# Kernel optimization log

Hardware: AMD Instinct MI355X
Metric: run time of the kernel (lower is better)

## Reference

```python
import jax, jax.numpy as jnp
from jax import lax
import numpy as np

N_HOS, N_TYPES, N_STRUCTS = 4, 16, 512
N_COMBOS = N_HOS * N_TYPES  # 64
HID = 1024
N_ITERS = 60  # fixed PDHG iterations (differentiable unrolled solver)


def setup_inputs() -> dict:
    key = jax.random.key(0)
    ks = jax.random.split(key, 8)
    X = jax.random.uniform(ks[0], (2048, N_HOS, N_TYPES), dtype=jnp.float32)
    # sparse 0/1 structure matrix; guarantee each structure touches >=1 combo
    S = (jax.random.uniform(ks[1], (N_COMBOS, N_STRUCTS)) < 0.08).astype(jnp.float32)
    cols = jnp.arange(N_STRUCTS)
    S = S.at[cols % N_COMBOS, cols].set(1.0)
    # MLP params (He-ish init)
    W1 = jax.random.normal(ks[2], (N_COMBOS, HID), dtype=jnp.float32) * (2.0 / N_COMBOS) ** 0.5
    b1 = jnp.zeros((HID,), jnp.float32)
    W2 = jax.random.normal(ks[3], (HID, HID), dtype=jnp.float32) * (2.0 / HID) ** 0.5
    b2 = jnp.zeros((HID,), jnp.float32)
    W3 = jax.random.normal(ks[4], (HID, N_STRUCTS), dtype=jnp.float32) * (2.0 / HID) ** 0.5
    b3 = jnp.zeros((N_STRUCTS,), jnp.float32)
    return {"X": X, "W1": W1, "b1": b1, "W2": W2, "b2": b2,
            "W3": W3, "b3": b3, "S": S, "batch_size": 2048}


def nn_forward(X, W1, b1, W2, b2, W3, b3):
    # torch loop applies act_fun after EVERY layer, including the last
    Z = X.reshape(X.shape[0], -1)                 # [B, n_hos*n_types]
    Z = jax.nn.relu(Z @ W1 + b1)
    Z = jax.nn.relu(Z @ W2 + b2)
    Z = jax.nn.relu(Z @ W3 + b3)                  # [B, n_structures]
    return Z


def solve_lp(S, W, B, Z, n_iters=N_ITERS):
    """Batched solve of: max_x W.x - ||x - Z||_2  s.t. x >= 0, S x <= B.
    PDHG (Chambolle-Pock) on  min_x f(x) + i{Kx <= c},
    f(x) = -W.x + ||x - Z||_2,  K = [S; -I],  c = [B; 0].
    Same optimization problem as the CvxpyLayer, solved by a fixed-iteration
    batched primal-dual method (differentiable via unrolling)."""
    batch, n = Z.shape
    m = S.shape[0]

    # ||K||_2 via power iteration on K^T K = S^T S + I (constant wrt params)
    def pow_step(v, _):
        v2 = S.T @ (S @ v) + v
        return v2 / jnp.linalg.norm(v2), None
    v0 = jnp.full((n,), 1.0 / np.sqrt(n), Z.dtype)
    v, _ = lax.scan(pow_step, v0, None, length=30)
    L = jnp.sqrt(jnp.vdot(v, S.T @ (S @ v) + v))
    L = lax.stop_gradient(L)
    tau = 0.9 / L
    sigma = 0.9 / L

    c = jnp.concatenate([B, jnp.zeros_like(Z)], axis=-1)  # [B, m+n]

    def Kx(x):
        return jnp.concatenate([x @ S.T, -x], axis=-1)    # [B, m+n]

    def KTy(y):
        return y[:, :m] @ S - y[:, m:]                    # [B, n]

    def prox_f(v):
        # argmin_x 1/(2 tau) ||x - v||^2 - W.x + ||x - Z||_2
        u = v + tau * W
        d = u - Z
        nrm = jnp.linalg.norm(d, axis=-1, keepdims=True)
        scale = jnp.maximum(1.0 - tau / jnp.maximum(nrm, 1e-12), 0.0)
        return Z + scale * d

    def step(carry, _):
        x, xbar, y = carry
        y = jnp.maximum(y + sigma * (Kx(xbar) - c), 0.0)
        x_new = prox_f(x - tau * KTy(y))
        xbar = 2.0 * x_new - x
        return (x_new, xbar, y), None

    x0 = jnp.zeros_like(Z)
    y0 = jnp.zeros((batch, m + n), Z.dtype)
    (x, _, _), _ = lax.scan(step, (x0, x0, y0), None, length=n_iters)
    return x


def reference(X, W1, b1, W2, b2, W3, b3, S, batch_size):
    Z = nn_forward(X, W1, b1, W2, b2, W3, b3)     # [B, n_structures]
    W = jnp.ones_like(Z)                          # weights w = 1 (as in torch)
    B = X.reshape(batch_size, -1)                 # capacities b
    return solve_lp(S, W, B, Z)
```

## Files before the change

### kernel.cpp

```cpp
#include <hip/hip_runtime.h>


typedef _Float16 half8 __attribute__((ext_vector_type(8)));
typedef __fp16 fp16x2 __attribute__((ext_vector_type(2)));
typedef __fp16 fp16x4 __attribute__((ext_vector_type(4)));
typedef float floatx4 __attribute__((ext_vector_type(4)));
typedef float floatx2 __attribute__((ext_vector_type(2)));

#define BATCH 2048
#define NITERS 60
#define XBS 520
#define YLS 72

typedef const __attribute__((address_space(1))) unsigned int* gptr_as1;
typedef __attribute__((address_space(3))) unsigned int* lptr_as3;
__device__ __forceinline__ void gl_lds16(const _Float16* g, _Float16* s) {
    __builtin_amdgcn_global_load_lds((gptr_as1)g, (lptr_as3)s, 16, 0, 0);
}
__device__ __forceinline__ floatx2 pmax0(floatx2 a) {
    return __builtin_elementwise_max(a, floatx2{0.f, 0.f});
}

template <int CTRL>
__device__ __forceinline__ float dpp_addf(float x) {
    int y = __builtin_amdgcn_update_dpp(0, __builtin_bit_cast(int, x), CTRL, 0xf, 0xf, true);
    return x + __builtin_bit_cast(float, y);
}
__device__ __forceinline__ float sum16(float x) {
    x = dpp_addf<0xB1>(x);
    x = dpp_addf<0x4E>(x);
    x = dpp_addf<0x124>(x);
    x = dpp_addf<0x128>(x);
    return x;
}
__device__ __forceinline__ float sum64(float x) {
    x = sum16(x);
    x += __builtin_bit_cast(float, __builtin_amdgcn_ds_swizzle(__builtin_bit_cast(int, x), 0x401F));
    x += __shfl_xor(x, 32, 64);
    return x;
}

__device__ void power_64(const float* __restrict__ S, float* __restrict__ tau_g) {
    __shared__ unsigned long long rowm[64][8];
    __shared__ float G[64][65];
    __shared__ float wl[64], pg[4][64];
    int t = threadIdx.x, wv = t >> 6, ln = t & 63;
    for (int rr = 0; rr < 16; rr++) {
        int r = wv * 16 + rr;
        float v[8];
#pragma unroll
        for (int e = 0; e < 8; e++) v[e] = S[r * 512 + e * 64 + ln];
#pragma unroll
        for (int e = 0; e < 8; e++) {
            unsigned long long m = __ballot(v[e] != 0.f);
            if (ln == 0) rowm[r][e] = m;
        }
    }
    __syncthreads();
    for (int k = 0; k < 16; k++) {
        int idx = t * 16 + k;
        int i = idx >> 6, j = idx & 63;
        int cnt = 0;
#pragma unroll
        for (int e = 0; e < 8; e++) cnt += __popcll(rowm[i][e] & rowm[j][e]);
        G[i][j] = (float)cnt;
    }
    if (wv == 0) {
        int cnt = 0;
#pragma unroll
        for (int e = 0; e < 8; e++) cnt += __popcll(rowm[ln][e]);
        wl[ln] = (float)cnt * 0.044194173824159216f;
    }
    __syncthreads();
    for (int s = 0; s < 30; s++) {
        float a = 0.f;
#pragma unroll
        for (int jj = 0; jj < 16; jj++) {
            int j = wv * 16 + jj;
            a += G[ln][j] * wl[j];
        }
        pg[wv][ln] = a;
        __syncthreads();
        if (wv == 0) {
            float g = (pg[0][ln] + pg[1][ln]) + (pg[2][ln] + pg[3][ln]);
            float wi = wl[ln];
            float s1 = sum64(wi * g);
            float s2 = sum64(wi * wi);
            float n = sqrtf(s1 + 2.f * s2 + 1.f);
            wl[ln] = (g + wi) / n;
        }
        __syncthreads();
    }
    if (wv == 0) {
        float wi = wl[ln];
        float s2 = sum64(wi * wi);
        if (ln == 0) tau_g[0] = 0.9f / sqrtf(s2 + 1.f);
    }
}

__global__ __launch_bounds__(256) void prep(
    const float* __restrict__ X, _Float16* __restrict__ Xh,
    const float* __restrict__ W1, _Float16* __restrict__ W1t,
    const float* __restrict__ W2, _Float16* __restrict__ W2t,
    const float* __restrict__ W3, _Float16* __restrict__ W3t,
    const float* __restrict__ S, _Float16* __restrict__ s1f,
    _Float16* __restrict__ s2f) {
    __shared__ float tile[32][33];
    int tid = threadIdx.x;
    int bid = blockIdx.x;
    if (bid < 512) {
        int i = bid * 256 + tid;
        Xh[i] = (_Float16)X[i];
        return;
    }
    bid -= 512;
    if (bid < 1600) {
        const float* W; _Float16* Wt; int K, N, b;
        if (bid < 64)        { W = W1; Wt = W1t; K = 64;   N = 1024; b = bid; }
        else if (bid < 1088) { W = W2; Wt = W2t; K = 1024; N = 1024; b = bid - 64; }
        else                 { W = W3; Wt = W3t; K = 1024; N = 512;  b = bid - 1088; }
        int nbx = N / 32;
        int n0 = (b % nbx) * 32, k0 = (b / nbx) * 32;
        int tx = tid & 31, ty = tid >> 5;
#pragma unroll
        for (int i = 0; i < 4; i++)
            tile[ty + i * 8][tx] = W[(size_t)(k0 + ty + i * 8) * N + n0 + tx];
        __syncthreads();
#pragma unroll
        for (int i = 0; i < 4; i++)
            Wt[(size_t)(n0 + ty + i * 8) * K + k0 + tx] = (_Float16)tile[tx][ty + i * 8];
        return;
    }
    bid -= 1600;
    int i = bid * 256 + tid;
    if (i < 4 * 16 * 64 * 8) {
        int j = i & 7, lane = (i >> 3) & 63, kk = (i >> 9) & 15, wc = i >> 13;
        int p = kk * 32 + (lane >> 4) * 8 + j;
        int lmc = (p & 127) >> 3, tc = p & 7;
        int c = (p >> 7) * 128 + tc * 16 + lmc;
        int m = wc * 16 + (lane & 15);
        s1f[i] = (_Float16)S[m * 512 + c];
    } else {
        int i2 = i - 4 * 16 * 64 * 8;
        int j = i2 & 7, lane = (i2 >> 3) & 63, c = (i2 >> 9) & 1,
            tt = (i2 >> 10) & 7, wc = i2 >> 13;
        int kc = c * 32 + (lane >> 4) * 8 + j;
        int n = wc * 128 + tt * 16 + (lane & 15);
        s2f[i2] = (_Float16)S[kc * 512 + n];
    }
}

__global__ __launch_bounds__(256) void gemm_relu(
    const _Float16* __restrict__ A, const _Float16* __restrict__ Wt,
    const float* __restrict__ bias, _Float16* __restrict__ outh,
    float* __restrict__ outf, int N, int K,
    const float* __restrict__ Sp, float* __restrict__ tau_g) {
    __shared__ __align__(16) _Float16 As[128 * 32];
    __shared__ __align__(16) _Float16 Bs[64 * 32];
    int tid = threadIdx.x;
    int bm = blockIdx.y * 128;
    int bn = blockIdx.x * 64;
    if (bn >= N) {
        if (blockIdx.y == 0 && Sp) power_64(Sp, tau_g);
        return;
    }
    int w = tid >> 6, l = tid & 63;
    int wr = w >> 1, wc = w & 1;
    int lm = l & 15, q = l >> 4;
    floatx4 acc[4][2] = {};

    int sr = l >> 2;
    int sc = (l & 3) * 8;
    const _Float16* ag0 = A + (size_t)(bm + w * 32 + sr) * K + sc;
    const _Float16* ag1 = A + (size_t)(bm + w * 32 + 16 + sr) * K + sc;
    _Float16* as0 = &As[(w * 32) * 32];
    _Float16* as1 = &As[(w * 32 + 16) * 32];
    const _Float16* bg = Wt + (size_t)(bn + w * 16 + sr) * K + sc;
    _Float16* bs = &Bs[(w * 16) * 32];

    for (int k0 = 0; k0 < K; k0 += 32) {
        gl_lds16(ag0 + k0, as0);
        gl_lds16(ag1 + k0, as1);
        gl_lds16(bg + k0, bs);
        __syncthreads();
        half8 af[4], bf[2];
#pragma unroll
        for (int mt = 0; mt < 4; mt++)
            af[mt] = *(const half8*)&As[(wr * 64 + mt * 16 + lm) * 32 + q * 8];
#pragma unroll
        for (int nt = 0; nt < 2; nt++)
            bf[nt] = *(const half8*)&Bs[(wc * 32 + nt * 16 + lm) * 32 + q * 8];
#pragma unroll
        for (int mt = 0; mt < 4; mt++)
#pragma unroll
            for (int nt = 0; nt < 2; nt++)
                acc[mt][nt] = __builtin_amdgcn_mfma_f32_16x16x32_f16(
                    af[mt], bf[nt], acc[mt][nt], 0, 0, 0);
        __syncthreads();
    }
#pragma unroll
    for (int nt = 0; nt < 2; nt++) {
        int col = bn + wc * 32 + nt * 16 + lm;
        float bv = bias[col];
#pragma unroll
        for (int mt = 0; mt < 4; mt++) {
#pragma unroll
            for (int v = 0; v < 4; v++) {
                int row = bm + wr * 64 + mt * 16 + q * 4 + v;
                float val = fmaxf(acc[mt][nt][v] + bv, 0.f);
                if (outh) outh[(size_t)row * N + col] = (_Float16)val;
                else      outf[(size_t)row * N + col] = val;
            }
        }
    }
}

__global__ __launch_bounds__(512, 2) void pdhg_mfma(
    const float* __restrict__ Zb, const float* __restrict__ Xf,
    const _Float16* __restrict__ s1f, const _Float16* __restrict__ s2f,
    const float* __restrict__ tau_p, float* __restrict__ out) {
    __shared__ __align__(16) _Float16 xb_d[16 * XBS];
    __shared__ __align__(16) _Float16 yl_d[16 * YLS];
    __shared__ __align__(16) float red[16][8];
    int tid = threadIdx.x;
    int wave = tid >> 6, p = wave >> 1, s = wave & 1;
    int l = tid & 63, lm = l & 15, q = l >> 4;
    int b0 = blockIdx.x * 8;
    bool act = (q < 2);

    half8 s1[16], s2[4][2];
#pragma unroll
    for (int k = 0; k < 16; k++)
        s1[k] = *(const half8*)&s1f[((p * 16 + k) * 64 + l) * 8];
#pragma unroll
    for (int tt = 0; tt < 4; tt++)
#pragma unroll
        for (int c = 0; c < 2; c++)
            s2[tt][c] = *(const half8*)&s2f[(((p * 8 + s * 4 + tt) * 2 + c) * 64 + l) * 8];

    floatx2 z2[2][4], x2[2][4], xb2[2][4], yh2[2][4], d2[2][4];
    floatx2 ylo2[2], Bc2[2];
    floatx4 a1p[4] = {};
    floatx4 acc2[4] = {};
    float tau = tau_p[0];
    float sig = tau;
#pragma unroll
    for (int vp = 0; vp < 2; vp++) {
        int r0 = b0 + ((q * 4 + 2 * vp) & 7);
        int r1 = b0 + ((q * 4 + 2 * vp + 1) & 7);
        Bc2[vp] = floatx2{Xf[r0 * 64 + p * 16 + lm], Xf[r1 * 64 + p * 16 + lm]};
        ylo2[vp] = floatx2{0.f, 0.f};
#pragma unroll
        for (int tt = 0; tt < 4; tt++) {
            int cc = p * 128 + (s * 4 + tt) * 16 + lm;
            z2[vp][tt] = floatx2{Zb[(size_t)r0 * 512 + cc], Zb[(size_t)r1 * 512 + cc]};
            x2[vp][tt] = floatx2{0.f, 0.f};
            xb2[vp][tt] = floatx2{0.f, 0.f};
            yh2[vp][tt] = floatx2{0.f, 0.f};
        }
    }
    {
        half8 hz = {0, 0, 0, 0, 0, 0, 0, 0};
        for (int i = tid; i < (16 * XBS) / 8; i += 512)
            *(half8*)&xb_d[i * 8] = hz;
        for (int i = tid; i < 16 * YLS; i += 512)
            yl_d[i] = (_Float16)0.f;
    }
    __syncthreads();

#pragma unroll 1
    for (int it = 0; it < NITERS; ++it) {
#pragma unroll
        for (int k = 0; k < 16; k++) {
            half8 ad = *(const half8*)&xb_d[lm * XBS + k * 32 + q * 8];
            a1p[k & 3] = __builtin_amdgcn_mfma_f32_16x16x32_f16(ad, s1[k], a1p[k & 3], 0, 0, 0);
        }
        floatx4 a1 = (a1p[0] + a1p[1]) + (a1p[2] + a1p[3]);
#pragma unroll
        for (int vp = 0; vp < 2; vp++) {
            floatx2 av = (vp == 0) ? floatx2{a1.x, a1.y} : floatx2{a1.z, a1.w};
            floatx2 yv = pmax0(ylo2[vp] + sig * (av - Bc2[vp]));
            floatx2 dy = yv - ylo2[vp];
            ylo2[vp] = yv;
            if (act && vp == s) {
                fp16x2 pk = __builtin_amdgcn_cvt_pkrtz(dy.x, dy.y);
                int a0 = (q * 4 + 2 * vp) * YLS + p * 16 + lm;
                yl_d[a0] = (_Float16)pk[0];
                yl_d[a0 + YLS] = (_Float16)pk[1];
            }
        }
        __syncthreads();
        half8 a2d[2];
#pragma unroll
        for (int c = 0; c < 2; c++)
            a2d[c] = *(const half8*)&yl_d[lm * YLS + c * 32 + q * 8];
#pragma unroll
        for (int tt = 0; tt < 4; tt++)
#pragma unroll
            for (int c = 0; c < 2; c++)
                acc2[tt] = __builtin_amdgcn_mfma_f32_16x16x32_f16(a2d[c], s2[tt][c], acc2[tt], 0, 0, 0);
        floatx2 pn2[2] = {floatx2{0.f, 0.f}, floatx2{0.f, 0.f}};
#pragma unroll
        for (int vp = 0; vp < 2; vp++)
#pragma unroll
            for (int tt = 0; tt < 4; tt++) {
                floatx2 accp = (vp == 0) ? floatx2{acc2[tt].x, acc2[tt].y}
                                         : floatx2{acc2[tt].z, acc2[tt].w};
                yh2[vp][tt] = pmax0(yh2[vp][tt] - sig * xb2[vp][tt]);
                floatx2 kty = accp - yh2[vp][tt];
                floatx2 dd = (x2[vp][tt] - tau * kty) + (tau - z2[vp][tt]);
                d2[vp][tt] = dd;
                pn2[vp] += dd * dd;
            }
        float pn[4] = {pn2[0].x, pn2[0].y, pn2[1].x, pn2[1].y};
#pragma unroll
        for (int v = 0; v < 4; v++) pn[v] = sum16(pn[v]);
        if (lm == 0)
#pragma unroll
            for (int v = 0; v < 4; v++) red[q * 4 + v][wave] = pn[v];
        __syncthreads();
        floatx2 sc2[2];
#pragma unroll
        for (int vp = 0; vp < 2; vp++)
#pragma unroll
            for (int c = 0; c < 2; c++) {
                int v = 2 * vp + c;
                floatx4 r0 = *(const floatx4*)&red[q * 4 + v][0];
                floatx4 r1 = *(const floatx4*)&red[q * 4 + v][4];
                floatx4 rr = r0 + r1;
                float n2 = (rr.x + rr.y) + (rr.z + rr.w);
                float sv = fmaxf(1.f - tau * rsqrtf(fmaxf(n2, 1e-24f)), 0.f);
                if (c == 0) sc2[vp].x = sv; else sc2[vp].y = sv;
            }
#pragma unroll
        for (int vp = 0; vp < 2; vp++) {
#pragma unroll
            for (int tt = 0; tt < 4; tt++) {
                floatx2 xn = z2[vp][tt] + sc2[vp] * d2[vp][tt];
                floatx2 xbn = 2.f * xn - x2[vp][tt];
                d2[vp][tt] = xbn - xb2[vp][tt];
                x2[vp][tt] = xn;
                xb2[vp][tt] = xbn;
            }
            if (act) {
#pragma unroll
                for (int c = 0; c < 2; c++) {
                    fp16x2 p0 = __builtin_amdgcn_cvt_pkrtz(
                        (c == 0) ? d2[vp][0].x : d2[vp][0].y,
                        (c == 0) ? d2[vp][1].x : d2[vp][1].y);
                    fp16x2 p1 = __builtin_amdgcn_cvt_pkrtz(
                        (c == 0) ? d2[vp][2].x : d2[vp][2].y,
                        (c == 0) ? d2[vp][3].x : d2[vp][3].y);
                    fp16x4 hd = __builtin_shufflevector(p0, p1, 0, 1, 2, 3);
                    int v = 2 * vp + c;
                    *(fp16x4*)&xb_d[(q * 4 + v) * XBS + p * 128 + lm * 8 + s * 4] = hd;
                }
            }
        }
        __syncthreads();
    }
    if (act)
#pragma unroll
        for (int vp = 0; vp < 2; vp++)
#pragma unroll
            for (int tt = 0; tt < 4; tt++) {
                int cc = p * 128 + (s * 4 + tt) * 16 + lm;
                out[(size_t)(b0 + q * 4 + 2 * vp) * 512 + cc] = x2[vp][tt].x;
                out[(size_t)(b0 + q * 4 + 2 * vp + 1) * 512 + cc] = x2[vp][tt].y;
            }
}

extern "C" void kernel_launch(void* const* d_in, const int* in_sizes, int n_in,
                              void* d_out, int out_size, void* d_ws, size_t ws_size,
                              hipStream_t stream) {
    const float* X  = (const float*)d_in[0];
    const float* W1 = (const float*)d_in[1];
    const float* b1 = (const float*)d_in[2];
    const float* W2 = (const float*)d_in[3];
    const float* b2 = (const float*)d_in[4];
    const float* W3 = (const float*)d_in[5];
    const float* b3 = (const float*)d_in[6];
    const float* S  = (const float*)d_in[7];
    float* out = (float*)d_out;

    char* ws = (char*)d_ws;
    size_t off = 0;
    auto alloc = [&](size_t bytes) {
        void* p = ws + off;
        off += (bytes + 255) & ~(size_t)255;
        return p;
    };
    _Float16* Xh  = (_Float16*)alloc((size_t)BATCH * 64 * 2);
    _Float16* W1t = (_Float16*)alloc((size_t)64 * 1024 * 2);
    _Float16* W2t = (_Float16*)alloc((size_t)1024 * 1024 * 2);
    _Float16* W3t = (_Float16*)alloc((size_t)1024 * 512 * 2);
    _Float16* H1  = (_Float16*)alloc((size_t)BATCH * 1024 * 2);
    _Float16* H2  = (_Float16*)alloc((size_t)BATCH * 1024 * 2);
    float*    Zb  = (float*)alloc((size_t)BATCH * 512 * 4);
    _Float16* s1f = (_Float16*)alloc((size_t)4 * 16 * 64 * 8 * 2);
    _Float16* s2f = (_Float16*)alloc((size_t)4 * 8 * 2 * 64 * 8 * 2);
    float*    tau = (float*)alloc(256);

    hipLaunchKernelGGL(prep, dim3(2368), dim3(256), 0, stream,
                       X, Xh, W1, W1t, W2, W2t, W3, W3t, S, s1f, s2f);
    hipLaunchKernelGGL(gemm_relu, dim3(16, 16), dim3(256), 0, stream,
                       Xh, W1t, b1, H1, (float*)nullptr, 1024, 64,
                       (const float*)nullptr, (float*)nullptr);
    hipLaunchKernelGGL(gemm_relu, dim3(17, 16), dim3(256), 0, stream,
                       H1, W2t, b2, H2, (float*)nullptr, 1024, 1024, S, tau);
    hipLaunchKernelGGL(gemm_relu, dim3(8, 16), dim3(256), 0, stream,
                       H2, W3t, b3, (_Float16*)nullptr, Zb, 512, 1024,
                       (const float*)nullptr, (float*)nullptr);
    hipLaunchKernelGGL(pdhg_mfma, dim3(BATCH / 8), dim3(512), 0, stream,
                       Zb, X, s1f, s2f, tau, out);
}
```

Measured before the change: 231.2 us.

## Restructure PDHG kernel to four waves per block with full MFMA row use

The PDHG solver block shrinks from 8 waves to 4 waves (256 threads). Each wave now owns a full 128-column slice and computes all 8 second-stage MFMA tiles. Previously half the lanes in the 16-row MFMA tiles were idle. Now the 8 batch rows are replicated across lm&7 and every lane holds a floatx4 of useful work, with the S1 fragment layout permuted in prep to match. The change also precomputes tau-z and swaps a wave pair reduction for a shfl_xor. It trades fewer waves per block, and likely lower occupancy under launch_bounds(256,1), for less redundant work and a smaller LDS reduction.

```diff
diff --git a/kernel.cpp b/kernel.cpp
--- a/kernel.cpp
+++ b/kernel.cpp
@@ -16,9 +16,6 @@
 typedef __attribute__((address_space(3))) unsigned int* lptr_as3;
 __device__ __forceinline__ void gl_lds16(const _Float16* g, _Float16* s) {
     __builtin_amdgcn_global_load_lds((gptr_as1)g, (lptr_as3)s, 16, 0, 0);
-}
-__device__ __forceinline__ floatx2 pmax0(floatx2 a) {
-    return __builtin_elementwise_max(a, floatx2{0.f, 0.f});
 }
 
 template <int CTRL>
@@ -135,9 +132,11 @@
     int i = bid * 256 + tid;
     if (i < 4 * 16 * 64 * 8) {
         int j = i & 7, lane = (i >> 3) & 63, kk = (i >> 9) & 15, wc = i >> 13;
-        int p = kk * 32 + (lane >> 4) * 8 + j;
-        int lmc = (p & 127) >> 3, tc = p & 7;
-        int c = (p >> 7) * 128 + tc * 16 + lmc;
+        int pos = kk * 32 + (lane >> 4) * 8 + j;
+        int pp = pos >> 7, r = pos & 127;
+        int hh = r >> 6, r2 = r & 63;
+        int lmc = r2 >> 2, t3 = r2 & 3;
+        int c = pp * 128 + (hh * 4 + t3) * 16 + lmc;
         int m = wc * 16 + (lane & 15);
         s1f[i] = (_Float16)S[m * 512 + c];
     } else {
@@ -215,55 +214,57 @@
     }
 }
 
-__global__ __launch_bounds__(512, 2) void pdhg_mfma(
+__global__ __launch_bounds__(256, 1) void pdhg_mfma(
     const float* __restrict__ Zb, const float* __restrict__ Xf,
     const _Float16* __restrict__ s1f, const _Float16* __restrict__ s2f,
     const float* __restrict__ tau_p, float* __restrict__ out) {
-    __shared__ __align__(16) _Float16 xb_d[16 * XBS];
-    __shared__ __align__(16) _Float16 yl_d[16 * YLS];
-    __shared__ __align__(16) float red[16][8];
+    __shared__ __align__(16) _Float16 xb_d[8 * XBS];
+    __shared__ __align__(16) _Float16 yl_d[8 * YLS];
+    __shared__ __align__(16) float red[8][4];
     int tid = threadIdx.x;
-    int wave = tid >> 6, p = wave >> 1, s = wave & 1;
+    int p = tid >> 6;
     int l = tid & 63, lm = l & 15, q = l >> 4;
+    int lq = lm & 7;
+    int qa = q & 1;
+    int h = q >> 1;
     int b0 = blockIdx.x * 8;
-    bool act = (q < 2);
-
-    half8 s1[16], s2[4][2];
+
+    half8 s1[16], s2[8][2];
 #pragma unroll
     for (int k = 0; k < 16; k++)
         s1[k] = *(const half8*)&s1f[((p * 16 + k) * 64 + l) * 8];
 #pragma unroll
-    for (int tt = 0; tt < 4; tt++)
+    for (int u = 0; u < 8; u++)
 #pragma unroll
         for (int c = 0; c < 2; c++)
-            s2[tt][c] = *(const half8*)&s2f[(((p * 8 + s * 4 + tt) * 2 + c) * 64 + l) * 8];
-
-    floatx2 z2[2][4], x2[2][4], xb2[2][4], yh2[2][4], d2[2][4];
-    floatx2 ylo2[2], Bc2[2];
+            s2[u][c] = *(const half8*)&s2f[(((p * 8 + u) * 2 + c) * 64 + l) * 8];
+
+    floatx4 z4[4], tz4[4], x4[4], xb4[4], yh4[4], d4[4];
+    floatx4 ylo = {}, Bc;
     floatx4 a1p[4] = {};
-    floatx4 acc2[4] = {};
+    floatx4 acc2[8] = {};
+    const floatx4 zero4 = {0.f, 0.f, 0.f, 0.f};
     float tau = tau_p[0];
     float sig = tau;
-#pragma unroll
-    for (int vp = 0; vp < 2; vp++) {
-        int r0 = b0 + ((q * 4 + 2 * vp) & 7);
-        int r1 = b0 + ((q * 4 + 2 * vp + 1) & 7);
-        Bc2[vp] = floatx2{Xf[r0 * 64 + p * 16 + lm], Xf[r1 * 64 + p * 16 + lm]};
-        ylo2[vp] = floatx2{0.f, 0.f};
-#pragma unroll
-        for (int tt = 0; tt < 4; tt++) {
-            int cc = p * 128 + (s * 4 + tt) * 16 + lm;
-            z2[vp][tt] = floatx2{Zb[(size_t)r0 * 512 + cc], Zb[(size_t)r1 * 512 + cc]};
-            x2[vp][tt] = floatx2{0.f, 0.f};
-            xb2[vp][tt] = floatx2{0.f, 0.f};
-            yh2[vp][tt] = floatx2{0.f, 0.f};
-        }
+
+#pragma unroll
+    for (int v = 0; v < 4; v++)
+        Bc[v] = Xf[(b0 + qa * 4 + v) * 64 + p * 16 + lm];
+#pragma unroll
+    for (int t = 0; t < 4; t++) {
+#pragma unroll
+        for (int v = 0; v < 4; v++) {
+            float zz = Zb[(size_t)(b0 + qa * 4 + v) * 512 + p * 128 + (h * 4 + t) * 16 + lm];
+            z4[t][v] = zz;
+            tz4[t][v] = tau - zz;
+        }
+        x4[t] = zero4; xb4[t] = zero4; yh4[t] = zero4;
     }
     {
         half8 hz = {0, 0, 0, 0, 0, 0, 0, 0};
-        for (int i = tid; i < (16 * XBS) / 8; i += 512)
+        for (int i = tid; i < (8 * XBS) / 8; i += 256)
             *(half8*)&xb_d[i * 8] = hz;
-        for (int i = tid; i < 16 * YLS; i += 512)
+        for (int i = tid; i < 8 * YLS; i += 256)
             yl_d[i] = (_Float16)0.f;
     }
     __syncthreads();
@@ -272,102 +273,76 @@
     for (int it = 0; it < NITERS; ++it) {
 #pragma unroll
         for (int k = 0; k < 16; k++) {
-            half8 ad = *(const half8*)&xb_d[lm * XBS + k * 32 + q * 8];
+            half8 ad = *(const half8*)&xb_d[lq * XBS + k * 32 + q * 8];
             a1p[k & 3] = __builtin_amdgcn_mfma_f32_16x16x32_f16(ad, s1[k], a1p[k & 3], 0, 0, 0);
         }
         floatx4 a1 = (a1p[0] + a1p[1]) + (a1p[2] + a1p[3]);
-#pragma unroll
-        for (int vp = 0; vp < 2; vp++) {
-            floatx2 av = (vp == 0) ? floatx2{a1.x, a1.y} : floatx2{a1.z, a1.w};
-            floatx2 yv = pmax0(ylo2[vp] + sig * (av - Bc2[vp]));
-            floatx2 dy = yv - ylo2[vp];
-            ylo2[vp] = yv;
-            if (act && vp == s) {
-                fp16x2 pk = __builtin_amdgcn_cvt_pkrtz(dy.x, dy.y);
-                int a0 = (q * 4 + 2 * vp) * YLS + p * 16 + lm;
-                yl_d[a0] = (_Float16)pk[0];
-                yl_d[a0 + YLS] = (_Float16)pk[1];
-            }
+        floatx4 yv = __builtin_elementwise_max(ylo + sig * (a1 - Bc), zero4);
+        floatx4 dy = yv - ylo;
+        ylo = yv;
+        if (q < 2) {
+#pragma unroll
+            for (int v = 0; v < 4; v++)
+                yl_d[(q * 4 + v) * YLS + p * 16 + lm] = (_Float16)dy[v];
         }
         __syncthreads();
         half8 a2d[2];
 #pragma unroll
         for (int c = 0; c < 2; c++)
-            a2d[c] = *(const half8*)&yl_d[lm * YLS + c * 32 + q * 8];
-#pragma unroll
-        for (int tt = 0; tt < 4; tt++)
+            a2d[c] = *(const half8*)&yl_d[lq * YLS + c * 32 + q * 8];
+#pragma unroll
+        for (int u = 0; u < 8; u++)
 #pragma unroll
             for (int c = 0; c < 2; c++)
-                acc2[tt] = __builtin_amdgcn_mfma_f32_16x16x32_f16(a2d[c], s2[tt][c], acc2[tt], 0, 0, 0);
-        floatx2 pn2[2] = {floatx2{0.f, 0.f}, floatx2{0.f, 0.f}};
-#pragma unroll
-        for (int vp = 0; vp < 2; vp++)
-#pragma unroll
-            for (int tt = 0; tt < 4; tt++) {
-                floatx2 accp = (vp == 0) ? floatx2{acc2[tt].x, acc2[tt].y}
-                                         : floatx2{acc2[tt].z, acc2[tt].w};
-                yh2[vp][tt] = pmax0(yh2[vp][tt] - sig * xb2[vp][tt]);
-                floatx2 kty = accp - yh2[vp][tt];
-                floatx2 dd = (x2[vp][tt] - tau * kty) + (tau - z2[vp][tt]);
-                d2[vp][tt] = dd;
-                pn2[vp] += dd * dd;
-            }
-        float pn[4] = {pn2[0].x, pn2[0].y, pn2[1].x, pn2[1].y};
+                acc2[u] = __builtin_amdgcn_mfma_f32_16x16x32_f16(a2d[c], s2[u][c], acc2[u], 0, 0, 0);
+        floatx4 pn = {};
+#pragma unroll
+        for (int t = 0; t < 4; t++) {
+            floatx4 accs = h ? acc2[t + 4] : acc2[t];
+            yh4[t] = __builtin_elementwise_max(yh4[t] - sig * xb4[t], zero4);
+            floatx4 kty = accs - yh4[t];
+            floatx4 dd = (x4[t] - tau * kty) + tz4[t];
+            d4[t] = dd;
+            pn += dd * dd;
+        }
 #pragma unroll
         for (int v = 0; v < 4; v++) pn[v] = sum16(pn[v]);
-        if (lm == 0)
-#pragma unroll
-            for (int v = 0; v < 4; v++) red[q * 4 + v][wave] = pn[v];
-        __syncthreads();
-        floatx2 sc2[2];
-#pragma unroll
-        for (int vp = 0; vp < 2; vp++)
-#pragma unroll
-            for (int c = 0; c < 2; c++) {
-                int v = 2 * vp + c;
-                floatx4 r0 = *(const floatx4*)&red[q * 4 + v][0];
-                floatx4 r1 = *(const floatx4*)&red[q * 4 + v][4];
-                floatx4 rr = r0 + r1;
-                float n2 = (rr.x + rr.y) + (rr.z + rr.w);
-                float sv = fmaxf(1.f - tau * rsqrtf(fmaxf(n2, 1e-24f)), 0.f);
-                if (c == 0) sc2[vp].x = sv; else sc2[vp].y = sv;
-            }
-#pragma unroll
-        for (int vp = 0; vp < 2; vp++) {
-#pragma unroll
-            for (int tt = 0; tt < 4; tt++) {
-                floatx2 xn = z2[vp][tt] + sc2[vp] * d2[vp][tt];
-                floatx2 xbn = 2.f * xn - x2[vp][tt];
-                d2[vp][tt] = xbn - xb2[vp][tt];
-                x2[vp][tt] = xn;
-                xb2[vp][tt] = xbn;
-            }
-            if (act) {
-#pragma unroll
-                for (int c = 0; c < 2; c++) {
-                    fp16x2 p0 = __builtin_amdgcn_cvt_pkrtz(
-                        (c == 0) ? d2[vp][0].x : d2[vp][0].y,
-                        (c == 0) ? d2[vp][1].x : d2[vp][1].y);
-                    fp16x2 p1 = __builtin_amdgcn_cvt_pkrtz(
-                        (c == 0) ? d2[vp][2].x : d2[vp][2].y,
-                        (c == 0) ? d2[vp][3].x : d2[vp][3].y);
-                    fp16x4 hd = __builtin_shufflevector(p0, p1, 0, 1, 2, 3);
-                    int v = 2 * vp + c;
-                    *(fp16x4*)&xb_d[(q * 4 + v) * XBS + p * 128 + lm * 8 + s * 4] = hd;
-                }
-            }
-        }
-        __syncthreads();
-    }
-    if (act)
-#pragma unroll
-        for (int vp = 0; vp < 2; vp++)
-#pragma unroll
-            for (int tt = 0; tt < 4; tt++) {
-                int cc = p * 128 + (s * 4 + tt) * 16 + lm;
-                out[(size_t)(b0 + q * 4 + 2 * vp) * 512 + cc] = x2[vp][tt].x;
-                out[(size_t)(b0 + q * 4 + 2 * vp + 1) * 512 + cc] = x2[vp][tt].y;
-            }
+#pragma unroll
+        for (int v = 0; v < 4; v++) pn[v] += __shfl_xor(pn[v], 32, 64);
+        if (lm == 0 && q < 2) {
+#pragma unroll
+            for (int v = 0; v < 4; v++) red[q * 4 + v][p] = pn[v];
+        }
+        __syncthreads();
+        floatx4 sv;
+#pragma unroll
+        for (int v = 0; v < 4; v++) {
+            floatx4 rr = *(const floatx4*)&red[qa * 4 + v][0];
+            float n2 = (rr.x + rr.y) + (rr.z + rr.w);
+            sv[v] = fmaxf(1.f - tau * rsqrtf(fmaxf(n2, 1e-24f)), 0.f);
+        }
+#pragma unroll
+        for (int t = 0; t < 4; t++) {
+            floatx4 xn = z4[t] + sv * d4[t];
+            floatx4 xbn = 2.f * xn - x4[t];
+            d4[t] = xbn - xb4[t];
+            x4[t] = xn;
+            xb4[t] = xbn;
+        }
+#pragma unroll
+        for (int v = 0; v < 4; v++) {
+            fp16x2 p0 = __builtin_amdgcn_cvt_pkrtz(d4[0][v], d4[1][v]);
+            fp16x2 p1 = __builtin_amdgcn_cvt_pkrtz(d4[2][v], d4[3][v]);
+            fp16x4 hd = __builtin_shufflevector(p0, p1, 0, 1, 2, 3);
+            *(fp16x4*)&xb_d[(qa * 4 + v) * XBS + p * 128 + h * 64 + lm * 4] = hd;
+        }
+        __syncthreads();
+    }
+#pragma unroll
+    for (int t = 0; t < 4; t++)
+#pragma unroll
+        for (int v = 0; v < 4; v++)
+            out[(size_t)(b0 + qa * 4 + v) * 512 + p * 128 + (h * 4 + t) * 16 + lm] = x4[t][v];
 }
 
 extern "C" void kernel_launch(void* const* d_in, const int* in_sizes, int n_in,
@@ -411,6 +386,6 @@
     hipLaunchKernelGGL(gemm_relu, dim3(8, 16), dim3(256), 0, stream,
                        H2, W3t, b3, (_Float16*)nullptr, Zb, 512, 1024,
                        (const float*)nullptr, (float*)nullptr);
-    hipLaunchKernelGGL(pdhg_mfma, dim3(BATCH / 8), dim3(512), 0, stream,
+    hipLaunchKernelGGL(pdhg_mfma, dim3(BATCH / 8), dim3(256), 0, stream,
                        Zb, X, s1f, s2f, tau, out);
 }
```

New measurement: 208.2 us. 10.0% less time.
